# Performance work log

Measured on AMD Instinct MI355X. Metric: run time of the kernel, lower is better.

## Reference

```python
import jax, jax.numpy as jnp
import numpy as np

# init config (from init_kwargs)
EMBED_DIM = 32          # D
N_PIXELS = 8192         # N
KERNEL_BANDWIDTH = 0.5
STEP_SIZE = 0.5
NB_ITERATIONS = 5


def setup_inputs() -> dict:
    key = jax.random.key(0)
    # embeddings live in a bounded ball (margin-based loss) -> scale down so
    # exp(bw * <x_i, x_j>) stays numerically tame, like trained embeddings.
    x_in = jax.random.normal(key, (EMBED_DIM, N_PIXELS), dtype=jnp.float32) * 0.1
    return {"x_in": x_in}


def reference(x_in):
    """Mean-shift iterations on D x N embeddings.

    Each step: K = exp(bw * x^T x)  (N x N, symmetric)
               x <- step * x @ (K / colsum(K)) + (1 - step) * x
    which is exactly x @ (step * K @ inv(diag(K^T 1)) + (1-step) * I)
    from the original torch code, without materializing diag/inverse/eye.
    """
    step = jnp.float32(STEP_SIZE)
    bw = jnp.float32(KERNEL_BANDWIDTH)

    def body(x, _):
        kernel = jnp.exp(bw * (x.T @ x))          # [N, N]
        deg = kernel.sum(axis=0)                  # column sums d_j, [N]
        x_new = step * (x @ kernel) / deg + (1.0 - step) * x  # [D, N]
        return x_new, None

    x_out, _ = jax.lax.scan(body, x_in, None, length=NB_ITERATIONS)
    return x_out
```

## Files before the change

### kernel.cpp

```cpp
#include <hip/hip_runtime.h>
#include <hip/hip_bf16.h>
#include <math.h>


typedef short bf16x8 __attribute__((ext_vector_type(8)));
typedef float f32x16 __attribute__((ext_vector_type(16)));
typedef int v2i __attribute__((ext_vector_type(2)));

#define NPIX 8192
#define DIM 32
#define NITER 5
#define SCH 16
#define CHUNK (NPIX / SCH)
#define HALF 256
#define HALVES (CHUNK / HALF)
#define WAVES 8
#define ALPHA 0.8493219f

#if __has_builtin(__builtin_amdgcn_exp2f)
#define EXP2(x) __builtin_amdgcn_exp2f(x)
#else
#define EXP2(x) exp2f(x)
#endif

__device__ __forceinline__ void glds16(const uint4* g, uint4* l) {
#if __has_builtin(__builtin_amdgcn_global_load_lds)
    __builtin_amdgcn_global_load_lds((const __attribute__((address_space(1))) void*)g,
                                     (__attribute__((address_space(3))) void*)l,
                                     16, 0, 0);
#else
    *l = *g;
#endif
}

__device__ inline unsigned cvtpk(float lo, float hi) {
    unsigned r;
    asm("v_cvt_pk_bf16_f32 %0, %1, %2" : "=v"(r) : "v"(lo), "v"(hi));
    return r;
}

__device__ inline void swap32(unsigned a, unsigned b, unsigned& x, unsigned& y) {
#if __has_builtin(__builtin_amdgcn_permlane32_swap)
    v2i r = __builtin_amdgcn_permlane32_swap((int)a, (int)b, false, false);
    x = (unsigned)r.x;
    y = (unsigned)r.y;
#else
    unsigned bs = __shfl_xor(b, 32);
    unsigned as = __shfl_xor(a, 32);
    int hi = (int)(threadIdx.x & 63) >> 5;
    x = hi ? bs : a;
    y = hi ? b : as;
#endif
}

__device__ inline unsigned short f2bf(float f) {
    unsigned u = __float_as_uint(f);
    unsigned r = (u + 0x7FFFu + ((u >> 16) & 1u)) >> 16;
    return (unsigned short)r;
}

__device__ inline unsigned pk2(float a, float b) {
    return (unsigned)f2bf(a) | ((unsigned)f2bf(b) << 16);
}

__device__ inline float bfl(unsigned u) { return __uint_as_float(u << 16); }
__device__ inline float bfh(unsigned u) { return __uint_as_float(u & 0xFFFF0000u); }

union U4 { uint4 q; bf16x8 v; };

__global__ __launch_bounds__(512, 4) void k_ms(const unsigned short* __restrict__ kq,
                                               const unsigned short* __restrict__ vv,
                                               unsigned short* __restrict__ party,
                                               float* __restrict__ partd) {
    __shared__ uint4 sm[4096];
    const int tid = threadIdx.x;
    const int lane = tid & 63;
    const int lo = lane & 31, hi = lane >> 5;
    const int wv = tid >> 6;
    const int wbase = tid & ~63;
    const int jblk = blockIdx.x * WAVES + wv;
    const int chunk = blockIdx.y;

    const uint4* kq4 = (const uint4*)kq;
    const uint4* vv4 = (const uint4*)vv;

    U4 q0, q1;
    q0.q = kq4[jblk * 128 + lane];
    q1.q = kq4[jblk * 128 + 64 + lane];

    U4 ones;
    ones.q = make_uint4(0x3F803F80u, 0x3F803F80u, 0x3F803F80u, 0x3F803F80u);

    f32x16 z16;
#pragma unroll
    for (int r = 0; r < 16; ++r) z16[r] = 0.f;
    f32x16 y = z16;
    f32x16 dg16 = z16;

    const uint4* gk = kq4 + (size_t)chunk * CHUNK * 4;
    const uint4* gv = vv4 + (size_t)chunk * CHUNK * 4;

    auto STAGE = [&](int h, int b) {
        const uint4* gkh = gk + h * (HALF * 4);
        const uint4* gvh = gv + h * (HALF * 4);
        uint4* dK = sm + b * 2048 + wbase;
#pragma unroll
        for (int r = 0; r < 2; ++r) {
            glds16(gkh + r * 512 + tid, dK + r * 512);
            glds16(gvh + r * 512 + tid, dK + 1024 + r * 512);
        }
    };

    STAGE(0, 0);

    for (int h = 0; h < HALVES; ++h) {
        __builtin_amdgcn_s_barrier();
        if (h + 1 < HALVES) {
            STAGE(h + 1, (h + 1) & 1);
            asm volatile("s_waitcnt vmcnt(4)" ::: "memory");
        } else {
            asm volatile("s_waitcnt vmcnt(0)" ::: "memory");
        }
        __builtin_amdgcn_s_barrier();

        const uint4* bK = sm + ((h & 1) << 11);
        const uint4* bV = bK + 1024;
#pragma unroll
        for (int t = 0; t < HALF / 32; ++t) {
            U4 ka0, ka1, vb0, vb1;
            ka0.q = bK[t * 128 + lane];
            ka1.q = bK[t * 128 + 64 + lane];
            vb0.q = bV[t * 128 + lane];
            vb1.q = bV[t * 128 + 64 + lane];

            f32x16 s;
            s = __builtin_amdgcn_mfma_f32_32x32x16_bf16(ka0.v, q0.v, z16, 0, 0, 0);
            s = __builtin_amdgcn_mfma_f32_32x32x16_bf16(ka1.v, q1.v, s, 0, 0, 0);
            float p[16];
#pragma unroll
            for (int r = 0; r < 16; ++r) p[r] = EXP2(s[r]);

#pragma unroll
            for (int ks = 0; ks < 2; ++ks) {
                const float* pb = p + ks * 8;
                unsigned a0 = cvtpk(pb[0], pb[1]);
                unsigned a1 = cvtpk(pb[2], pb[3]);
                unsigned b0 = cvtpk(pb[4], pb[5]);
                unsigned b1 = cvtpk(pb[6], pb[7]);
                unsigned w01, w45, w23, w67;
                swap32(a0, b0, w01, w45);
                swap32(a1, b1, w23, w67);
                U4 pa;
                pa.q = make_uint4(w01, w23, w45, w67);
                y = __builtin_amdgcn_mfma_f32_32x32x16_bf16(
                        pa.v, (ks ? vb1.v : vb0.v), y, 0, 0, 0);
                dg16 = __builtin_amdgcn_mfma_f32_32x32x16_bf16(
                        pa.v, ones.v, dg16, 0, 0, 0);
            }
        }
    }

    unsigned short* yrow = party + ((size_t)chunk * NPIX + (size_t)jblk * 32) * 32;
    float* drow = partd + (size_t)chunk * NPIX + (size_t)jblk * 32;
#pragma unroll
    for (int r = 0; r < 16; ++r) {
        int jr = (r & 3) + 8 * (r >> 2) + 4 * hi;
        yrow[(size_t)jr * 32 + lo] = f2bf(y[r]);
        if (lo == 0) drow[jr] = dg16[r];
    }
}

__global__ __launch_bounds__(256) void k_prep(const float* __restrict__ xin,
                                              float* __restrict__ xm,
                                              unsigned short* __restrict__ kq,
                                              unsigned short* __restrict__ vv) {
    const int j = blockIdx.x * 256 + threadIdx.x;
    float xv[DIM];
#pragma unroll
    for (int d = 0; d < DIM; ++d) xv[d] = xin[(size_t)d * NPIX + j];

    float4* xmr = (float4*)(xm + (size_t)j * DIM);
#pragma unroll
    for (int q = 0; q < 8; ++q)
        xmr[q] = make_float4(xv[4*q], xv[4*q+1], xv[4*q+2], xv[4*q+3]);

    uint4* kq4 = (uint4*)kq;
#pragma unroll
    for (int ks = 0; ks < 2; ++ks)
#pragma unroll
        for (int h = 0; h < 2; ++h) {
            const int b = ks * 16 + h * 8;
            kq4[(j >> 5) * 128 + ks * 64 + h * 32 + (j & 31)] =
                make_uint4(pk2(xv[b+0]*ALPHA, xv[b+1]*ALPHA), pk2(xv[b+2]*ALPHA, xv[b+3]*ALPHA),
                           pk2(xv[b+4]*ALPHA, xv[b+5]*ALPHA), pk2(xv[b+6]*ALPHA, xv[b+7]*ALPHA));
        }

    const int vbase = (j >> 5) * 1024 + ((j >> 4) & 1) * 512 + ((j >> 3) & 1) * 256 + (j & 7);
#pragma unroll
    for (int d = 0; d < DIM; ++d) vv[vbase + d * 8] = f2bf(xv[d]);
}

__global__ __launch_bounds__(256) void k_upd(const unsigned short* __restrict__ party,
                                             const float* __restrict__ partd,
                                             const float* __restrict__ xm,
                                             float* __restrict__ xm_next,
                                             unsigned short* __restrict__ kq,
                                             unsigned short* __restrict__ vv,
                                             float* __restrict__ out,
                                             int last) {
    const int t = blockIdx.x * 256 + threadIdx.x;
    const int j = t >> 2, q = t & 3;

    float ys[8];
#pragma unroll
    for (int e = 0; e < 8; ++e) ys[e] = 0.f;
    float dg = 0.f;
    for (int c = 0; c < SCH; ++c) {
        uint4 u = *(const uint4*)(party + ((size_t)c * NPIX + j) * 32 + q * 8);
        ys[0] += bfl(u.x); ys[1] += bfh(u.x);
        ys[2] += bfl(u.y); ys[3] += bfh(u.y);
        ys[4] += bfl(u.z); ys[5] += bfh(u.z);
        ys[6] += bfl(u.w); ys[7] += bfh(u.w);
        dg += partd[(size_t)c * NPIX + j];
    }
    const float inv = 0.5f / dg;

    const float4* xr = (const float4*)(xm + (size_t)j * DIM + q * 8);
    float4 v0 = xr[0], v1 = xr[1];
    float xn[8];
    xn[0] = fmaf(ys[0], inv, 0.5f * v0.x);
    xn[1] = fmaf(ys[1], inv, 0.5f * v0.y);
    xn[2] = fmaf(ys[2], inv, 0.5f * v0.z);
    xn[3] = fmaf(ys[3], inv, 0.5f * v0.w);
    xn[4] = fmaf(ys[4], inv, 0.5f * v1.x);
    xn[5] = fmaf(ys[5], inv, 0.5f * v1.y);
    xn[6] = fmaf(ys[6], inv, 0.5f * v1.z);
    xn[7] = fmaf(ys[7], inv, 0.5f * v1.w);

    if (last) {
#pragma unroll
        for (int e = 0; e < 8; ++e) out[(size_t)(q * 8 + e) * NPIX + j] = xn[e];
        return;
    }

    float4* xw = (float4*)(xm_next + (size_t)j * DIM + q * 8);
    xw[0] = make_float4(xn[0], xn[1], xn[2], xn[3]);
    xw[1] = make_float4(xn[4], xn[5], xn[6], xn[7]);

    ((uint4*)kq)[(j >> 5) * 128 + (q >> 1) * 64 + (q & 1) * 32 + (j & 31)] =
        make_uint4(pk2(xn[0]*ALPHA, xn[1]*ALPHA), pk2(xn[2]*ALPHA, xn[3]*ALPHA),
                   pk2(xn[4]*ALPHA, xn[5]*ALPHA), pk2(xn[6]*ALPHA, xn[7]*ALPHA));

    const int vbase = (j >> 5) * 1024 + ((j >> 4) & 1) * 512 + ((j >> 3) & 1) * 256 + (j & 7);
#pragma unroll
    for (int e = 0; e < 8; ++e) vv[vbase + (q * 8 + e) * 8] = f2bf(xn[e]);
}

extern "C" void kernel_launch(void* const* d_in, const int* in_sizes, int n_in,
                              void* d_out, int out_size, void* d_ws, size_t ws_size,
                              hipStream_t stream) {
    const float* x_in = (const float*)d_in[0];
    float* out = (float*)d_out;

    const size_t nd = (size_t)NPIX * DIM;
    float* xmA = (float*)d_ws;
    float* xmB = xmA + nd;
    unsigned short* party = (unsigned short*)(xmB + nd);
    float* partd = (float*)(party + (size_t)SCH * NPIX * 32);
    unsigned short* kq = (unsigned short*)(partd + (size_t)SCH * NPIX);
    unsigned short* vv = kq + nd;

    k_prep<<<NPIX / 256, 256, 0, stream>>>(x_in, xmA, kq, vv);

    for (int it = 0; it < NITER; ++it) {
        const int last = (it == NITER - 1);
        k_ms<<<dim3(NPIX / (32 * WAVES), SCH), 512, 0, stream>>>(kq, vv, party, partd);
        k_upd<<<(NPIX * 4) / 256, 256, 0, stream>>>(party, partd, xmA, xmB, kq, vv, out, last);
        float* t = xmA; xmA = xmB; xmB = t;
    }
}
```

Before: 109.6 us.

## Permute V layout to drop permlane swaps and widen update kernel parallelism

The bf16 V operand is stored in a permuted row order (vslot) that matches the P accumulator's natural register layout. This lets the inner loop pack exp values straight into the MFMA A operand without permlane32 swaps. Separately, the update kernel now uses 8 threads per pixel instead of 4, each handling 4 dims with narrower loads. The first change saves VALU work in the hot loop; the second doubles the thread count of a small kernel, and both depend on the permuted layout being correct.

```diff
diff --git a/kernel.cpp b/kernel.cpp
--- a/kernel.cpp
+++ b/kernel.cpp
@@ -5,7 +5,6 @@
 
 typedef short bf16x8 __attribute__((ext_vector_type(8)));
 typedef float f32x16 __attribute__((ext_vector_type(16)));
-typedef int v2i __attribute__((ext_vector_type(2)));
 
 #define NPIX 8192
 #define DIM 32
@@ -39,20 +38,6 @@
     return r;
 }
 
-__device__ inline void swap32(unsigned a, unsigned b, unsigned& x, unsigned& y) {
-#if __has_builtin(__builtin_amdgcn_permlane32_swap)
-    v2i r = __builtin_amdgcn_permlane32_swap((int)a, (int)b, false, false);
-    x = (unsigned)r.x;
-    y = (unsigned)r.y;
-#else
-    unsigned bs = __shfl_xor(b, 32);
-    unsigned as = __shfl_xor(a, 32);
-    int hi = (int)(threadIdx.x & 63) >> 5;
-    x = hi ? bs : a;
-    y = hi ? b : as;
-#endif
-}
-
 __device__ inline unsigned short f2bf(float f) {
     unsigned u = __float_as_uint(f);
     unsigned r = (u + 0x7FFFu + ((u >> 16) & 1u)) >> 16;
@@ -65,6 +50,11 @@
 
 __device__ inline float bfl(unsigned u) { return __uint_as_float(u << 16); }
 __device__ inline float bfh(unsigned u) { return __uint_as_float(u & 0xFFFF0000u); }
+
+__device__ inline int vslot(int i) {
+    return (i >> 5) * 1024 + ((i >> 4) & 1) * 512 + ((i >> 2) & 1) * 256
+         + (i & 3) + 4 * ((i >> 3) & 1);
+}
 
 union U4 { uint4 q; bf16x8 v; };
 
@@ -143,15 +133,9 @@
 #pragma unroll
             for (int ks = 0; ks < 2; ++ks) {
                 const float* pb = p + ks * 8;
-                unsigned a0 = cvtpk(pb[0], pb[1]);
-                unsigned a1 = cvtpk(pb[2], pb[3]);
-                unsigned b0 = cvtpk(pb[4], pb[5]);
-                unsigned b1 = cvtpk(pb[6], pb[7]);
-                unsigned w01, w45, w23, w67;
-                swap32(a0, b0, w01, w45);
-                swap32(a1, b1, w23, w67);
                 U4 pa;
-                pa.q = make_uint4(w01, w23, w45, w67);
+                pa.q = make_uint4(cvtpk(pb[0], pb[1]), cvtpk(pb[2], pb[3]),
+                                  cvtpk(pb[4], pb[5]), cvtpk(pb[6], pb[7]));
                 y = __builtin_amdgcn_mfma_f32_32x32x16_bf16(
                         pa.v, (ks ? vb1.v : vb0.v), y, 0, 0, 0);
                 dg16 = __builtin_amdgcn_mfma_f32_32x32x16_bf16(
@@ -195,7 +179,7 @@
                            pk2(xv[b+4]*ALPHA, xv[b+5]*ALPHA), pk2(xv[b+6]*ALPHA, xv[b+7]*ALPHA));
         }
 
-    const int vbase = (j >> 5) * 1024 + ((j >> 4) & 1) * 512 + ((j >> 3) & 1) * 256 + (j & 7);
+    const int vbase = vslot(j);
 #pragma unroll
     for (int d = 0; d < DIM; ++d) vv[vbase + d * 8] = f2bf(xv[d]);
 }
@@ -209,51 +193,41 @@
                                              float* __restrict__ out,
                                              int last) {
     const int t = blockIdx.x * 256 + threadIdx.x;
-    const int j = t >> 2, q = t & 3;
-
-    float ys[8];
-#pragma unroll
-    for (int e = 0; e < 8; ++e) ys[e] = 0.f;
+    const int j = t >> 3, q = t & 7;
+
+    float ys[4] = {0.f, 0.f, 0.f, 0.f};
     float dg = 0.f;
     for (int c = 0; c < SCH; ++c) {
-        uint4 u = *(const uint4*)(party + ((size_t)c * NPIX + j) * 32 + q * 8);
+        uint2 u = *(const uint2*)(party + ((size_t)c * NPIX + j) * 32 + q * 4);
         ys[0] += bfl(u.x); ys[1] += bfh(u.x);
         ys[2] += bfl(u.y); ys[3] += bfh(u.y);
-        ys[4] += bfl(u.z); ys[5] += bfh(u.z);
-        ys[6] += bfl(u.w); ys[7] += bfh(u.w);
         dg += partd[(size_t)c * NPIX + j];
     }
     const float inv = 0.5f / dg;
 
-    const float4* xr = (const float4*)(xm + (size_t)j * DIM + q * 8);
-    float4 v0 = xr[0], v1 = xr[1];
-    float xn[8];
-    xn[0] = fmaf(ys[0], inv, 0.5f * v0.x);
-    xn[1] = fmaf(ys[1], inv, 0.5f * v0.y);
-    xn[2] = fmaf(ys[2], inv, 0.5f * v0.z);
-    xn[3] = fmaf(ys[3], inv, 0.5f * v0.w);
-    xn[4] = fmaf(ys[4], inv, 0.5f * v1.x);
-    xn[5] = fmaf(ys[5], inv, 0.5f * v1.y);
-    xn[6] = fmaf(ys[6], inv, 0.5f * v1.z);
-    xn[7] = fmaf(ys[7], inv, 0.5f * v1.w);
+    float4 v = *(const float4*)(xm + (size_t)j * DIM + q * 4);
+    float xn[4];
+    xn[0] = fmaf(ys[0], inv, 0.5f * v.x);
+    xn[1] = fmaf(ys[1], inv, 0.5f * v.y);
+    xn[2] = fmaf(ys[2], inv, 0.5f * v.z);
+    xn[3] = fmaf(ys[3], inv, 0.5f * v.w);
 
     if (last) {
 #pragma unroll
-        for (int e = 0; e < 8; ++e) out[(size_t)(q * 8 + e) * NPIX + j] = xn[e];
+        for (int e = 0; e < 4; ++e) out[(size_t)(q * 4 + e) * NPIX + j] = xn[e];
         return;
     }
 
-    float4* xw = (float4*)(xm_next + (size_t)j * DIM + q * 8);
-    xw[0] = make_float4(xn[0], xn[1], xn[2], xn[3]);
-    xw[1] = make_float4(xn[4], xn[5], xn[6], xn[7]);
-
-    ((uint4*)kq)[(j >> 5) * 128 + (q >> 1) * 64 + (q & 1) * 32 + (j & 31)] =
-        make_uint4(pk2(xn[0]*ALPHA, xn[1]*ALPHA), pk2(xn[2]*ALPHA, xn[3]*ALPHA),
-                   pk2(xn[4]*ALPHA, xn[5]*ALPHA), pk2(xn[6]*ALPHA, xn[7]*ALPHA));
-
-    const int vbase = (j >> 5) * 1024 + ((j >> 4) & 1) * 512 + ((j >> 3) & 1) * 256 + (j & 7);
-#pragma unroll
-    for (int e = 0; e < 8; ++e) vv[vbase + (q * 8 + e) * 8] = f2bf(xn[e]);
+    *(float4*)(xm_next + (size_t)j * DIM + q * 4) =
+        make_float4(xn[0], xn[1], xn[2], xn[3]);
+
+    const int ks = q >> 2, hh = (q >> 1) & 1;
+    ((uint2*)kq)[((size_t)(j >> 5) * 128 + ks * 64 + hh * 32 + (j & 31)) * 2 + (q & 1)] =
+        make_uint2(pk2(xn[0]*ALPHA, xn[1]*ALPHA), pk2(xn[2]*ALPHA, xn[3]*ALPHA));
+
+    const int vbase = vslot(j);
+#pragma unroll
+    for (int e = 0; e < 4; ++e) vv[vbase + (q * 4 + e) * 8] = f2bf(xn[e]);
 }
 
 extern "C" void kernel_launch(void* const* d_in, const int* in_sizes, int n_in,
@@ -275,7 +249,7 @@
     for (int it = 0; it < NITER; ++it) {
         const int last = (it == NITER - 1);
         k_ms<<<dim3(NPIX / (32 * WAVES), SCH), 512, 0, stream>>>(kq, vv, party, partd);
-        k_upd<<<(NPIX * 4) / 256, 256, 0, stream>>>(party, partd, xmA, xmB, kq, vv, out, last);
+        k_upd<<<(NPIX * 8) / 256, 256, 0, stream>>>(party, partd, xmA, xmB, kq, vv, out, last);
         float* t = xmA; xmA = xmB; xmB = t;
     }
 }
```

Measured after the change: 106.5 us. 1.03x faster.
